# Performance work log

Hardware: AMD Instinct MI355X
Metric: run time of the kernel (lower is better)

The kernel has to match this reference:

```python
import jax, jax.numpy as jnp
import numpy as np

E, N, D, LOAD = 8, 8192, 1024, 16384

def setup_inputs() -> dict:
    key = jax.random.key(0)
    k1, k2 = jax.random.split(key)
    in_flows_data = jax.random.normal(k1, (E, N, D), dtype=jnp.float32)
    in_flows_tag = jax.random.randint(k2, (E, N), 0, LOAD, dtype=jnp.int64)
    return {"in_flows_data": in_flows_data, "in_flows_tag": in_flows_tag, "load": LOAD}

def reference(in_flows_data, in_flows_tag, load):
    # GatherRouter.combine (reduction='add', sparse=False):
    # concat all routed flows along token dim, then scatter-add by tag
    # into an output of `load` token slots.
    e, n, d = in_flows_data.shape
    data = in_flows_data.reshape(e * n, d)   # torch.cat(in_flows_data, dim=0)
    tags = in_flows_tag.reshape(e * n)       # torch.cat(in_flows_tag, dim=0)
    # zeros(load, d).scatter_(0, tags_expanded, data, reduce='add')
    out_flow_data = jax.ops.segment_sum(data, tags, num_segments=load)
    return out_flow_data
```

## Files before the change

kernel.cpp:

```cpp
#include <hip/hip_runtime.h>

#define D_CONST    1024
#define CAP        64

__global__ void gr_build_index(const int* __restrict__ tags,
                               int* __restrict__ counts,
                               int* __restrict__ idx,
                               int* __restrict__ pos_arr,
                               int total) {
    int i = blockIdx.x * blockDim.x + threadIdx.x;
    if (i >= total) return;
    int t = tags[i];
    int pos = atomicAdd(&counts[t], 1);
    pos_arr[i] = pos;
    if (pos < CAP) idx[t * CAP + pos] = i;
}

__global__ void __launch_bounds__(256)
gr_gather_sum(const float* __restrict__ data,
              const int* __restrict__ counts,
              const int* __restrict__ idx,
              float* __restrict__ out) {
    const int r   = blockIdx.x;
    const int tid = threadIdx.x;
    int cnt = counts[r];
    if (cnt > CAP) cnt = CAP;
    const int* __restrict__ rowlist = idx + r * CAP;
    const int col = tid * 4;

    float4 acc = make_float4(0.f, 0.f, 0.f, 0.f);
    for (int j = 0; j < cnt; ++j) {
        int row = rowlist[j];
        const float4 v = *reinterpret_cast<const float4*>(
            data + (size_t)row * D_CONST + col);
        acc.x += v.x; acc.y += v.y; acc.z += v.z; acc.w += v.w;
    }
    *reinterpret_cast<float4*>(out + (size_t)r * D_CONST + col) = acc;
}

__global__ void gr_overflow(const float* __restrict__ data,
                            const int* __restrict__ tags,
                            const int* __restrict__ pos_arr,
                            float* __restrict__ out,
                            int total) {
    int i = blockIdx.x * blockDim.x + threadIdx.x;
    if (i >= total) return;
    if (pos_arr[i] < CAP) return;
    int t = tags[i];
    const float* src = data + (size_t)i * D_CONST;
    float* dst = out + (size_t)t * D_CONST;
    for (int c = 0; c < D_CONST; ++c) atomicAdd(&dst[c], src[c]);
}

__global__ void __launch_bounds__(256)
gr_atomic_scatter(const float* __restrict__ data,
                  const int* __restrict__ tags,
                  float* __restrict__ out,
                  int total) {
    const int row = blockIdx.x;
    if (row >= total) return;
    const int t = tags[row];
    const int col = threadIdx.x * 4;
    const float4 v = *reinterpret_cast<const float4*>(
        data + (size_t)row * D_CONST + col);
    float* dst = out + (size_t)t * D_CONST + col;
    atomicAdd(&dst[0], v.x);
    atomicAdd(&dst[1], v.y);
    atomicAdd(&dst[2], v.z);
    atomicAdd(&dst[3], v.w);
}

extern "C" void kernel_launch(void* const* d_in, const int* in_sizes, int n_in,
                              void* d_out, int out_size, void* d_ws, size_t ws_size,
                              hipStream_t stream) {
    const float* data = (const float*)d_in[0];
    const int*   tags = (const int*)d_in[1];

    const int total = in_sizes[1];
    const int load  = out_size / D_CONST;

    float* out = (float*)d_out;

    const size_t counts_bytes = (size_t)load * sizeof(int);
    const size_t pos_bytes    = (size_t)total * sizeof(int);
    const size_t idx_bytes    = (size_t)load * CAP * sizeof(int);
    const size_t needed       = counts_bytes + pos_bytes + idx_bytes;

    if (ws_size >= needed) {
        int* counts = (int*)d_ws;
        int* pos    = (int*)((char*)d_ws + counts_bytes);
        int* idx    = (int*)((char*)d_ws + counts_bytes + pos_bytes);

        hipMemsetAsync(counts, 0, counts_bytes, stream);

        gr_build_index<<<(total + 255) / 256, 256, 0, stream>>>(tags, counts, idx, pos, total);
        gr_gather_sum<<<load, 256, 0, stream>>>(data, counts, idx, out);
        gr_overflow<<<(total + 255) / 256, 256, 0, stream>>>(data, tags, pos, out, total);
    } else {
        hipMemsetAsync(out, 0, (size_t)out_size * sizeof(float), stream);
        gr_atomic_scatter<<<total, 256, 0, stream>>>(data, tags, out, total);
    }
}
```

Before: 394.6 us.

## Drop overflow kernel and pos array; unroll gather loop by four rows

Removes the per-token position array and the separate overflow kernel. Any tag with more than CAP entries is now handled inside the gather kernel by a linear scan over all tags. The gather loop loads four row indices at once with an int4 and issues four independent float4 loads to expose more memory-level parallelism. This saves one launch and one full pass over the tokens, but the fallback scan is very slow if overflow ever happens. With 65536 tokens spread over 16384 slots, overflow is very unlikely.

After: 391.8 us. No clear change (-0.7%).

```diff
diff --git a/kernel.cpp b/kernel.cpp
--- a/kernel.cpp
+++ b/kernel.cpp
@@ -6,13 +6,11 @@
 __global__ void gr_build_index(const int* __restrict__ tags,
                                int* __restrict__ counts,
                                int* __restrict__ idx,
-                               int* __restrict__ pos_arr,
                                int total) {
     int i = blockIdx.x * blockDim.x + threadIdx.x;
     if (i >= total) return;
     int t = tags[i];
     int pos = atomicAdd(&counts[t], 1);
-    pos_arr[i] = pos;
     if (pos < CAP) idx[t * CAP + pos] = i;
 }
 
@@ -20,36 +18,44 @@
 gr_gather_sum(const float* __restrict__ data,
               const int* __restrict__ counts,
               const int* __restrict__ idx,
-              float* __restrict__ out) {
+              const int* __restrict__ tags,
+              float* __restrict__ out,
+              int total) {
     const int r   = blockIdx.x;
-    const int tid = threadIdx.x;
-    int cnt = counts[r];
-    if (cnt > CAP) cnt = CAP;
-    const int* __restrict__ rowlist = idx + r * CAP;
-    const int col = tid * 4;
+    const int col = threadIdx.x * 4;
+    const int cnt = counts[r];
 
     float4 acc = make_float4(0.f, 0.f, 0.f, 0.f);
-    for (int j = 0; j < cnt; ++j) {
-        int row = rowlist[j];
-        const float4 v = *reinterpret_cast<const float4*>(
-            data + (size_t)row * D_CONST + col);
-        acc.x += v.x; acc.y += v.y; acc.z += v.z; acc.w += v.w;
+
+    if (cnt <= CAP) {
+        const int* __restrict__ rowlist = idx + r * CAP;
+        int j = 0;
+        for (; j + 4 <= cnt; j += 4) {
+            const int4 rw = *reinterpret_cast<const int4*>(rowlist + j);
+            const float4 v0 = *reinterpret_cast<const float4*>(data + (size_t)rw.x * D_CONST + col);
+            const float4 v1 = *reinterpret_cast<const float4*>(data + (size_t)rw.y * D_CONST + col);
+            const float4 v2 = *reinterpret_cast<const float4*>(data + (size_t)rw.z * D_CONST + col);
+            const float4 v3 = *reinterpret_cast<const float4*>(data + (size_t)rw.w * D_CONST + col);
+            acc.x += (v0.x + v1.x) + (v2.x + v3.x);
+            acc.y += (v0.y + v1.y) + (v2.y + v3.y);
+            acc.z += (v0.z + v1.z) + (v2.z + v3.z);
+            acc.w += (v0.w + v1.w) + (v2.w + v3.w);
+        }
+        for (; j < cnt; ++j) {
+            const int row = rowlist[j];
+            const float4 v = *reinterpret_cast<const float4*>(data + (size_t)row * D_CONST + col);
+            acc.x += v.x; acc.y += v.y; acc.z += v.z; acc.w += v.w;
+        }
+    } else {
+        for (int i = 0; i < total; ++i) {
+            if (tags[i] == r) {
+                const float4 v = *reinterpret_cast<const float4*>(data + (size_t)i * D_CONST + col);
+                acc.x += v.x; acc.y += v.y; acc.z += v.z; acc.w += v.w;
+            }
+        }
     }
+
     *reinterpret_cast<float4*>(out + (size_t)r * D_CONST + col) = acc;
-}
-
-__global__ void gr_overflow(const float* __restrict__ data,
-                            const int* __restrict__ tags,
-                            const int* __restrict__ pos_arr,
-                            float* __restrict__ out,
-                            int total) {
-    int i = blockIdx.x * blockDim.x + threadIdx.x;
-    if (i >= total) return;
-    if (pos_arr[i] < CAP) return;
-    int t = tags[i];
-    const float* src = data + (size_t)i * D_CONST;
-    float* dst = out + (size_t)t * D_CONST;
-    for (int c = 0; c < D_CONST; ++c) atomicAdd(&dst[c], src[c]);
 }
 
 __global__ void __launch_bounds__(256)
@@ -61,8 +67,7 @@
     if (row >= total) return;
     const int t = tags[row];
     const int col = threadIdx.x * 4;
-    const float4 v = *reinterpret_cast<const float4*>(
-        data + (size_t)row * D_CONST + col);
+    const float4 v = *reinterpret_cast<const float4*>(data + (size_t)row * D_CONST + col);
     float* dst = out + (size_t)t * D_CONST + col;
     atomicAdd(&dst[0], v.x);
     atomicAdd(&dst[1], v.y);
@@ -75,27 +80,21 @@
                               hipStream_t stream) {
     const float* data = (const float*)d_in[0];
     const int*   tags = (const int*)d_in[1];
-
     const int total = in_sizes[1];
     const int load  = out_size / D_CONST;
-
     float* out = (float*)d_out;
 
     const size_t counts_bytes = (size_t)load * sizeof(int);
-    const size_t pos_bytes    = (size_t)total * sizeof(int);
     const size_t idx_bytes    = (size_t)load * CAP * sizeof(int);
-    const size_t needed       = counts_bytes + pos_bytes + idx_bytes;
+    const size_t needed       = counts_bytes + idx_bytes;
 
     if (ws_size >= needed) {
         int* counts = (int*)d_ws;
-        int* pos    = (int*)((char*)d_ws + counts_bytes);
-        int* idx    = (int*)((char*)d_ws + counts_bytes + pos_bytes);
+        int* idx    = (int*)((char*)d_ws + counts_bytes);
 
         hipMemsetAsync(counts, 0, counts_bytes, stream);
-
-        gr_build_index<<<(total + 255) / 256, 256, 0, stream>>>(tags, counts, idx, pos, total);
-        gr_gather_sum<<<load, 256, 0, stream>>>(data, counts, idx, out);
-        gr_overflow<<<(total + 255) / 256, 256, 0, stream>>>(data, tags, pos, out, total);
+        gr_build_index<<<(total + 255) / 256, 256, 0, stream>>>(tags, counts, idx, total);
+        gr_gather_sum<<<load, 256, 0, stream>>>(data, counts, idx, tags, out, total);
     } else {
         hipMemsetAsync(out, 0, (size_t)out_size * sizeof(float), stream);
         gr_atomic_scatter<<<total, 256, 0, stream>>>(data, tags, out, total);
```
